# Kernel optimization log

Measured on AMD Instinct MI355X. Metric: run time of the kernel, lower is better.

The kernel has to match this reference:

```python
import jax, jax.numpy as jnp
import numpy as np

B, CIN, COUT, R = 8, 256, 256, 128  # H = W = R (required by the module's permute-then-conv structure)


def _init_linear(key, out_c, in_c):
    # mimic torch Conv2d(kernel=1) default init: uniform(-1/sqrt(fan_in), 1/sqrt(fan_in))
    k1, k2 = jax.random.split(key)
    bound = 1.0 / np.sqrt(in_c)
    W = jax.random.uniform(k1, (out_c, in_c), jnp.float32, -bound, bound)
    b = jax.random.uniform(k2, (out_c,), jnp.float32, -bound, bound)
    return W, b


def setup_inputs() -> dict:
    key = jax.random.key(0)
    keys = jax.random.split(key, 9)
    x = jax.random.normal(keys[0], (B, CIN, R, R), jnp.float32)
    Wr, br = _init_linear(keys[1], R, CIN)          # resize conv
    Wqw, bqw = _init_linear(keys[2], R, R)          # width-attn q (mixes over H axis, H==R)
    Wkw, bkw = _init_linear(keys[3], R, R)
    Wvw, bvw = _init_linear(keys[4], R, R)
    Wqh, bqh = _init_linear(keys[5], R, R)          # height-attn q (mixes over W axis, W==R)
    Wkh, bkh = _init_linear(keys[6], R, R)
    Wvh, bvh = _init_linear(keys[7], R, R)
    Wo, bo = _init_linear(keys[8], COUT, R)         # restore conv
    return dict(x=x, Wr=Wr, br=br, Wqw=Wqw, bqw=bqw, Wkw=Wkw, bkw=bkw, Wvw=Wvw, bvw=bvw,
                Wqh=Wqh, bqh=bqh, Wkh=Wkh, bkh=bkh, Wvh=Wvh, bvh=bvh, Wo=Wo, bo=bo)


def _csaa_forward(x, Wr, br, Wqw, bqw, Wkw, bkw, Wvw, bvw, Wqh, bqh, Wkh, bkh, Wvh, bvh, Wo, bo):
    # resize 1x1 conv: [B,CIN,H,W] -> [B,R,H,W]
    resized = jnp.einsum('oc,bchw->bohw', Wr, x) + br[None, :, None, None]

    # --- width-branch AxialAttention (height_dim=False) ---
    # permute(0,2,1,3): [B,R,H,W] -> [B,H,R,W]; 1x1 conv now mixes over the H axis (H==R)
    xp = jnp.transpose(resized, (0, 2, 1, 3))                      # [B,H,R,W]
    q = jnp.einsum('oh,bhrw->borw', Wqw, xp) + bqw[None, :, None, None]
    k = jnp.einsum('oh,bhrw->borw', Wkw, xp) + bkw[None, :, None, None]
    v = jnp.einsum('oh,bhrw->borw', Wvw, xp) + bvw[None, :, None, None]
    attn = jax.nn.softmax(jnp.einsum('borw,bouw->boru', q, k), axis=-1)  # [B,O,R,R]
    out = jnp.einsum('boru,bouw->borw', attn, v)                   # [B,O,R,W]
    w_attn = jnp.transpose(out, (0, 2, 1, 3))                      # [B,R,O,W] == [B,R,H,W]

    # --- height-branch AxialAttention (height_dim=True) ---
    # permute(0,3,1,2): [B,R,H,W] -> [B,W,R,H]; 1x1 conv mixes over the W axis (W==R)
    xp = jnp.transpose(w_attn, (0, 3, 1, 2))                       # [B,W,R,H]
    q = jnp.einsum('ow,bwrh->borh', Wqh, xp) + bqh[None, :, None, None]
    k = jnp.einsum('ow,bwrh->borh', Wkh, xp) + bkh[None, :, None, None]
    v = jnp.einsum('ow,bwrh->borh', Wvh, xp) + bvh[None, :, None, None]
    attn = jax.nn.softmax(jnp.einsum('borh,bouh->boru', q, k), axis=-1)  # [B,O,R,R]
    out = jnp.einsum('boru,bouh->borh', attn, v)                   # [B,O,R,H]
    h_attn = jnp.transpose(out, (0, 2, 3, 1))                      # [B,R,H,O] == [B,R,H,W]

    # restore 1x1 conv: [B,R,H,W] -> [B,COUT,H,W]
    return jnp.einsum('oc,bchw->bohw', Wo, h_attn) + bo[None, :, None, None]


def reference(x, Wr, br, Wqw, bqw, Wkw, bkw, Wvw, bvw, Wqh, bqh, Wkh, bkh, Wvh, bvh, Wo, bo):
    return _csaa_forward(x, Wr, br, Wqw, bqw, Wkw, bkw, Wvw, bvw,
                         Wqh, bqh, Wkh, bkh, Wvh, bvh, Wo, bo)
```

## Files before the change

kernel.cpp:

```cpp
#include <hip/hip_runtime.h>
#include <hip/hip_bf16.h>


typedef __attribute__((ext_vector_type(8))) short bf16x8;
typedef __attribute__((ext_vector_type(4))) float f32x4;

__device__ __forceinline__ short f2b(float f) {
    __hip_bfloat16 h = __float2bfloat16(f);
    short s; __builtin_memcpy(&s, &h, 2);
    return s;
}

__device__ __forceinline__ int swx(int row) { return (row ^ (row >> 3)) & 7; }
__device__ __forceinline__ int swzb(int row, int blk) {
    return (row << 7) + ((blk ^ swx(row)) << 3);
}

__device__ __forceinline__ void gload16(const void* g, void* l) {
    __builtin_amdgcn_global_load_lds(
        (const __attribute__((address_space(1))) void*)g,
        (__attribute__((address_space(3))) void*)l, 16, 0, 0);
}

__device__ __forceinline__ void mfma32x128(const short* __restrict__ SA,
                                           const short* __restrict__ SB,
                                           f32x4 (&acc)[2][8], int lane, int wr) {
    #pragma unroll
    for (int kk = 0; kk < 4; kk++) {
        const int kb = kk * 4 + (lane >> 4);
        bf16x8 a[2], b[8];
        #pragma unroll
        for (int mi = 0; mi < 2; mi++)
            a[mi] = *(const bf16x8*)&SA[swzb(wr + mi * 16 + (lane & 15), kb)];
        #pragma unroll
        for (int ni = 0; ni < 8; ni++)
            b[ni] = *(const bf16x8*)&SB[swzb(ni * 16 + (lane & 15), kb)];
        #pragma unroll
        for (int mi = 0; mi < 2; mi++)
            #pragma unroll
            for (int ni = 0; ni < 8; ni++)
                acc[mi][ni] = __builtin_amdgcn_mfma_f32_16x16x32_bf16(
                    a[mi], b[ni], acc[mi][ni], 0, 0, 0);
    }
}

__device__ __forceinline__ void mfma16x128(const short* __restrict__ SA,
                                           const short* __restrict__ SB,
                                           f32x4 (&acc)[8], int lane, int wr16) {
    #pragma unroll
    for (int kk = 0; kk < 4; kk++) {
        const int kb = kk * 4 + (lane >> 4);
        bf16x8 a = *(const bf16x8*)&SA[swzb(wr16 + (lane & 15), kb)];
        bf16x8 b[8];
        #pragma unroll
        for (int ni = 0; ni < 8; ni++)
            b[ni] = *(const bf16x8*)&SB[swzb(ni * 16 + (lane & 15), kb)];
        #pragma unroll
        for (int ni = 0; ni < 8; ni++)
            acc[ni] = __builtin_amdgcn_mfma_f32_16x16x32_bf16(
                a, b[ni], acc[ni], 0, 0, 0);
    }
}

__device__ __forceinline__ void stage_nf_bf16(const short* __restrict__ Bb,
                                              long long b_r, int k0,
                                              short* __restrict__ Bs, int t) {
    const int n8 = t & 15, kb = t >> 4;
    bf16x8 rk[8];
    #pragma unroll
    for (int i = 0; i < 8; i++)
        rk[i] = *(const bf16x8*)(Bb + (long long)(k0 + kb * 8 + i) * b_r + n8 * 8);
    #pragma unroll
    for (int j = 0; j < 8; j++) {
        bf16x8 col;
        #pragma unroll
        for (int i = 0; i < 8; i++) col[i] = rk[i][j];
        *(bf16x8*)&Bs[swzb(n8 * 8 + j, kb)] = col;
    }
}

__device__ __forceinline__ void stage_nf_f32(const float* __restrict__ Bb,
                                             long long b_r, int k0,
                                             short* __restrict__ Bs, int t) {
    const int n8 = t & 15, kb = t >> 4;
    bf16x8 rk[8];
    #pragma unroll
    for (int i = 0; i < 8; i++) {
        const float* s = Bb + (long long)(k0 + kb * 8 + i) * b_r + n8 * 8;
        float4 v0 = *(const float4*)s, v1 = *(const float4*)(s + 4);
        rk[i][0] = f2b(v0.x); rk[i][1] = f2b(v0.y);
        rk[i][2] = f2b(v0.z); rk[i][3] = f2b(v0.w);
        rk[i][4] = f2b(v1.x); rk[i][5] = f2b(v1.y);
        rk[i][6] = f2b(v1.z); rk[i][7] = f2b(v1.w);
    }
    #pragma unroll
    for (int j = 0; j < 8; j++) {
        bf16x8 col;
        #pragma unroll
        for (int i = 0; i < 8; i++) col[i] = rk[i][j];
        *(bf16x8*)&Bs[swzb(n8 * 8 + j, kb)] = col;
    }
}

__global__ __launch_bounds__(256)
void wprep(const float* __restrict__ Wr, const float* __restrict__ Wqw,
           const float* __restrict__ Wkw, const float* __restrict__ Wvw,
           const float* __restrict__ Wqh, const float* __restrict__ Wkh,
           const float* __restrict__ Wvh, const float* __restrict__ Wo,
           short* __restrict__ dst) {
    const int id = blockIdx.y;
    const float* W; int M, K, off;
    switch (id) {
        case 0: W = Wr;  M = 128; K = 256; off = 0;      break;
        case 1: W = Wqw; M = 128; K = 128; off = 32768;  break;
        case 2: W = Wkw; M = 128; K = 128; off = 49152;  break;
        case 3: W = Wvw; M = 128; K = 128; off = 65536;  break;
        case 4: W = Wqh; M = 128; K = 128; off = 81920;  break;
        case 5: W = Wkh; M = 128; K = 128; off = 98304;  break;
        case 6: W = Wvh; M = 128; K = 128; off = 114688; break;
        default: W = Wo; M = 256; K = 128; off = 131072; break;
    }
    int g = blockIdx.x * 256 + threadIdx.x;
    if (g >= (M * K) >> 3) return;
    int gpr = K >> 3;
    int row = g / gpr;
    int blk = g - row * gpr;
    int ks = blk >> 4, bi = blk & 15;
    int my = row >> 7, r = row & 127;
    int nks = K >> 7;
    const float* s = W + (long long)row * K + blk * 8;
    float4 v0 = *(const float4*)s, v1 = *(const float4*)(s + 4);
    bf16x8 ov;
    ov[0] = f2b(v0.x); ov[1] = f2b(v0.y); ov[2] = f2b(v0.z); ov[3] = f2b(v0.w);
    ov[4] = f2b(v1.x); ov[5] = f2b(v1.y); ov[6] = f2b(v1.z); ov[7] = f2b(v1.w);
    *(bf16x8*)(dst + off + (my * nks + ks) * 16384 + swzb(r, bi)) = ov;
}

__global__ __launch_bounds__(256)
void gemm_p1(const short* __restrict__ A0, const float* __restrict__ bias0,
             const float* __restrict__ Bsrc,
             long long b_z, long long b_x, long long b_r,
             short* __restrict__ C0,
             long long c_z, long long c_x, long long c_m) {
    __shared__ short As[16384];
    __shared__ short Bs[16384];
    const int t = threadIdx.x;
    const int lane = t & 63;
    const int wid = t >> 6;
    const int wr = wid * 32;
    const int bx = blockIdx.x, bz = blockIdx.z;

    f32x4 acc[2][8];
    #pragma unroll
    for (int mi = 0; mi < 2; mi++)
        #pragma unroll
        for (int ni = 0; ni < 8; ni++) acc[mi][ni] = (f32x4){0.f, 0.f, 0.f, 0.f};

    #pragma unroll
    for (int ks = 0; ks < 2; ks++) {
        if (ks) __syncthreads();
        stage_nf_f32(Bsrc + bz * b_z + bx * b_x, b_r, ks * 128, Bs, t);
        const short* Ai = A0 + ks * 16384;
        #pragma unroll
        for (int i = 0; i < 8; i++) {
            int q = wid * 8 + i;
            gload16(Ai + q * 512 + lane * 8, &As[q * 512]);
        }
        __syncthreads();
        mfma32x128(As, Bs, acc, lane, wr);
    }

    #pragma unroll
    for (int mi = 0; mi < 2; mi++)
        #pragma unroll
        for (int r = 0; r < 4; r++) {
            int row = wr + mi * 16 + (lane >> 4) * 4 + r;
            float bb = bias0[row];
            #pragma unroll
            for (int ni = 0; ni < 8; ni++) {
                int col = ni * 16 + (lane & 15);
                As[swzb(row, col >> 3) + (col & 7)] = f2b(acc[mi][ni][r] + bb);
            }
        }
    short* Cg = C0 + bz * c_z + bx * c_x;
    #pragma unroll
    for (int i = 0; i < 8; i++) {
        int idx = lane + i * 64;
        int row = wr + (idx >> 4), ch = idx & 15;
        *(bf16x8*)(Cg + (long long)row * c_m + ch * 8) =
            *(const bf16x8*)&As[swzb(row, ch)];
    }
}

template<int NW, int BMODE, bool F32OUT>
__global__ __launch_bounds__(256, 3)
void gemmw64(const short* __restrict__ A0, const short* __restrict__ A1,
             const short* __restrict__ A2,
             const float* __restrict__ bias0, const float* __restrict__ bias1,
             const float* __restrict__ bias2,
             const void* __restrict__ Bsrc, long long b_z, long long b_x,
             long long b_r,
             short* __restrict__ C0, short* __restrict__ C1,
             short* __restrict__ C2, float* __restrict__ Cf,
             long long c_z, long long c_x, long long c_m) {
    __shared__ short As[8192];
    __shared__ short Bs[16384];
    const int t = threadIdx.x;
    const int lane = t & 63;
    const int wid = t >> 6;
    const int wr16 = wid * 16;
    const int bx = blockIdx.x, my = blockIdx.y, bz = blockIdx.z;
    const int mbase = my * 64;

    if (BMODE == 0) {
        const short* Bb = (const short*)Bsrc + bz * b_z + bx * b_x;
        #pragma unroll
        for (int i = 0; i < 8; i++) {
            int q = wid * 8 + i;
            int row = q * 4 + (lane >> 4);
            gload16(Bb + (long long)row * b_r + (((lane & 15) ^ swx(row)) << 3),
                    &Bs[q * 512]);
        }
    } else {
        stage_nf_bf16((const short*)Bsrc + bz * b_z + bx * b_x, b_r, 0, Bs, t);
    }
    {
        const short* Ai = A0 + my * 8192;
        #pragma unroll
        for (int i = 0; i < 4; i++) {
            int q = wid * 4 + i;
            gload16(Ai + q * 512 + lane * 8, &As[q * 512]);
        }
    }
    __syncthreads();

    #pragma unroll
    for (int g = 0; g < NW; g++) {
        const float* bias = (g == 0) ? bias0 : (g == 1) ? bias1 : bias2;
        f32x4 acc[8];
        #pragma unroll
        for (int ni = 0; ni < 8; ni++) acc[ni] = (f32x4){0.f, 0.f, 0.f, 0.f};
        mfma16x128(As, Bs, acc, lane, wr16);

        if (F32OUT) {
            float* Cb = Cf + bz * c_z + bx * c_x;
            #pragma unroll
            for (int r = 0; r < 4; r++) {
                int row = mbase + wr16 + (lane >> 4) * 4 + r;
                float bb = bias[row];
                float* cp = Cb + (long long)row * c_m + (lane & 15);
                #pragma unroll
                for (int ni = 0; ni < 8; ni++)
                    cp[ni * 16] = acc[ni][r] + bb;
            }
        } else {
            #pragma unroll
            for (int r = 0; r < 4; r++) {
                int row = wr16 + (lane >> 4) * 4 + r;
                float bb = bias[mbase + row];
                #pragma unroll
                for (int ni = 0; ni < 8; ni++) {
                    int col = ni * 16 + (lane & 15);
                    As[swzb(row, col >> 3) + (col & 7)] = f2b(acc[ni][r] + bb);
                }
            }
            short* Cg = ((g == 0) ? C0 : (g == 1) ? C1 : C2)
                      + bz * c_z + bx * c_x;
            #pragma unroll
            for (int i = 0; i < 4; i++) {
                int idx = lane + i * 64;
                int row = wr16 + (idx >> 4), ch = idx & 15;
                *(bf16x8*)(Cg + (long long)(mbase + row) * c_m + ch * 8) =
                    *(const bf16x8*)&As[swzb(row, ch)];
            }
        }
        if (g + 1 < NW) {
            const short* Ai = ((g == 0) ? A1 : A2) + my * 8192;
            #pragma unroll
            for (int i = 0; i < 4; i++) {
                int q = wid * 4 + i;
                gload16(Ai + q * 512 + lane * 8, &As[q * 512]);
            }
            __syncthreads();
        }
    }
}

template<bool TEPI>
__global__ __launch_bounds__(256)
void attnk(const short* __restrict__ Q, const short* __restrict__ Kp,
           const short* __restrict__ V, short* __restrict__ O) {
    __shared__ short SA[16384];
    __shared__ short SB[16384];
    const int t = threadIdx.x;
    const int lane = t & 63;
    const int wid = t >> 6;
    const int wr = wid * 32;
    const long long poff = (long long)blockIdx.z * 2097152LL
                         + (long long)blockIdx.x * 16384LL;
    const short* Qb = Q + poff;
    const short* Kb = Kp + poff;
    const short* Vb = V + poff;
    short* Ob = O + (long long)blockIdx.z * 2097152LL + (long long)blockIdx.x * 128LL;

    #pragma unroll
    for (int i = 0; i < 8; i++) {
        int q = wid * 8 + i;
        int row = q * 4 + (lane >> 4);
        int sw = (((lane & 15) ^ swx(row)) << 3);
        gload16(Qb + row * 128 + sw, &SA[q * 512]);
        gload16(Kb + row * 128 + sw, &SB[q * 512]);
    }
    const int n8 = t & 15, kb = t >> 4;
    bf16x8 vk[8];
    #pragma unroll
    for (int i = 0; i < 8; i++)
        vk[i] = *(const bf16x8*)(Vb + (kb * 8 + i) * 128 + n8 * 8);
    __syncthreads();

    f32x4 acc[2][8];
    #pragma unroll
    for (int mi = 0; mi < 2; mi++)
        #pragma unroll
        for (int ni = 0; ni < 8; ni++) acc[mi][ni] = (f32x4){0.f, 0.f, 0.f, 0.f};
    mfma32x128(SA, SB, acc, lane, wr);

    float rs[2][4];
    #pragma unroll
    for (int mi = 0; mi < 2; mi++)
        #pragma unroll
        for (int r = 0; r < 4; r++) {
            float mx = acc[mi][0][r];
            #pragma unroll
            for (int ni = 1; ni < 8; ni++) mx = fmaxf(mx, acc[mi][ni][r]);
            #pragma unroll
            for (int d = 1; d < 16; d <<= 1) mx = fmaxf(mx, __shfl_xor(mx, d, 64));
            float s = 0.f;
            float p[8];
            #pragma unroll
            for (int ni = 0; ni < 8; ni++) {
                p[ni] = __expf(acc[mi][ni][r] - mx);
                s += p[ni];
            }
            #pragma unroll
            for (int d = 1; d < 16; d <<= 1) s += __shfl_xor(s, d, 64);
            rs[mi][r] = 1.f / s;
            int row = wr + mi * 16 + (lane >> 4) * 4 + r;
            #pragma unroll
            for (int ni = 0; ni < 8; ni++) {
                int col = ni * 16 + (lane & 15);
                SA[swzb(row, col >> 3) + (col & 7)] = f2b(p[ni]);
            }
        }
    __syncthreads();

    #pragma unroll
    for (int j = 0; j < 8; j++) {
        bf16x8 col;
        #pragma unroll
        for (int i = 0; i < 8; i++) col[i] = vk[i][j];
        *(bf16x8*)&SB[swzb(n8 * 8 + j, kb)] = col;
    }
    __syncthreads();

    f32x4 acc2[2][8];
    #pragma unroll
    for (int mi = 0; mi < 2; mi++)
        #pragma unroll
        for (int ni = 0; ni < 8; ni++) acc2[mi][ni] = (f32x4){0.f, 0.f, 0.f, 0.f};
    mfma32x128(SA, SB, acc2, lane, wr);

    if (!TEPI) {
        #pragma unroll
        for (int mi = 0; mi < 2; mi++)
            #pragma unroll
            for (int r = 0; r < 4; r++) {
                int row = wr + mi * 16 + (lane >> 4) * 4 + r;
                float rinv = rs[mi][r];
                #pragma unroll
                for (int ni = 0; ni < 8; ni++) {
                    int col = ni * 16 + (lane & 15);
                    SA[swzb(row, col >> 3) + (col & 7)] = f2b(acc2[mi][ni][r] * rinv);
                }
            }
        #pragma unroll
        for (int i = 0; i < 8; i++) {
            int idx = lane + i * 64;
            int row = wr + (idx >> 4), ch = idx & 15;
            *(bf16x8*)(Ob + (long long)row * 16384 + ch * 8) =
                *(const bf16x8*)&SA[swzb(row, ch)];
        }
    } else {
        __syncthreads();
        #pragma unroll
        for (int mi = 0; mi < 2; mi++)
            #pragma unroll
            for (int r = 0; r < 4; r++) {
                int row = wr + mi * 16 + (lane >> 4) * 4 + r;
                float rinv = rs[mi][r];
                #pragma unroll
                for (int ni = 0; ni < 8; ni++) {
                    int col = ni * 16 + (lane & 15);
                    SB[swzb(col, row >> 3) + (row & 7)] = f2b(acc2[mi][ni][r] * rinv);
                }
            }
        __syncthreads();
        #pragma unroll
        for (int i = 0; i < 8; i++) {
            int idx = t + i * 256;
            int row = idx >> 4, ch = idx & 15;
            *(bf16x8*)(Ob + (long long)row * 16384 + ch * 8) =
                *(const bf16x8*)&SB[swzb(row, ch)];
        }
    }
}

extern "C" void kernel_launch(void* const* d_in, const int* in_sizes, int n_in,
                              void* d_out, int out_size, void* d_ws, size_t ws_size,
                              hipStream_t stream) {
    const float* x   = (const float*)d_in[0];
    const float* Wr  = (const float*)d_in[1];
    const float* br  = (const float*)d_in[2];
    const float* Wqw = (const float*)d_in[3];
    const float* bqw = (const float*)d_in[4];
    const float* Wkw = (const float*)d_in[5];
    const float* bkw = (const float*)d_in[6];
    const float* Wvw = (const float*)d_in[7];
    const float* bvw = (const float*)d_in[8];
    const float* Wqh = (const float*)d_in[9];
    const float* bqh = (const float*)d_in[10];
    const float* Wkh = (const float*)d_in[11];
    const float* bkh = (const float*)d_in[12];
    const float* Wvh = (const float*)d_in[13];
    const float* bvh = (const float*)d_in[14];
    const float* Wo  = (const float*)d_in[15];
    const float* bo  = (const float*)d_in[16];
    float* out = (float*)d_out;
    (void)in_sizes; (void)n_in; (void)out_size; (void)ws_size;

    const long long U = 16777216LL;
    short* wsp = (short*)d_ws;
    short* s0 = wsp;
    short* s1 = wsp + U;
    short* s2 = wsp + 2 * U;
    short* s3 = wsp + 3 * U;
    short* wb = wsp + 4 * U;
    short* wWr  = wb;
    short* wWqw = wb + 32768;
    short* wWkw = wb + 49152;
    short* wWvw = wb + 65536;
    short* wWqh = wb + 81920;
    short* wWkh = wb + 98304;
    short* wWvh = wb + 114688;
    short* wWo  = wb + 131072;

    dim3 blk(256);

    wprep<<<dim3(16, 8), blk, 0, stream>>>(Wr, Wqw, Wkw, Wvw, Wqh, Wkh, Wvh, Wo, wb);

    gemm_p1<<<dim3(128, 1, 8), blk, 0, stream>>>(
        wWr, br, x, 4194304LL, 128LL, 16384LL,
        s0, 2097152LL, 128LL, 16384LL);

    gemmw64<3, 1, false><<<dim3(128, 2, 8), blk, 0, stream>>>(
        wWqw, wWkw, wWvw, bqw, bkw, bvw,
        s0, 2097152LL, 16384LL, 128LL,
        s1, s2, s3, nullptr, 2097152LL, 128LL, 16384LL);

    attnk<false><<<dim3(128, 1, 8), blk, 0, stream>>>(s1, s2, s3, s0);

    gemmw64<3, 0, false><<<dim3(128, 2, 8), blk, 0, stream>>>(
        wWqh, wWkh, wWvh, bqh, bkh, bvh,
        s0, 2097152LL, 16384LL, 128LL,
        s1, s2, s3, nullptr, 2097152LL, 128LL, 16384LL);

    attnk<true><<<dim3(128, 1, 8), blk, 0, stream>>>(s1, s2, s3, s0);

    gemmw64<1, 0, true><<<dim3(128, 4, 8), blk, 0, stream>>>(
        wWo, nullptr, nullptr, bo, nullptr, nullptr,
        s0, 2097152LL, 16384LL, 128LL,
        nullptr, nullptr, nullptr, out, 4194304LL, 128LL, 16384LL);
}
```

Before: 216.7 us.

## Read weights from global in MFMA fragment layout and split attention by query halves

Weights are pre-packed into an MFMA-fragment order so GEMM kernels load A operands directly from global/L2 into registers instead of staging them through LDS, halving LDS use and allowing higher occupancy (launch bounds 4). The QKV projection kernel now assigns one weight per grid-y block with a 128-row tile instead of looping over weights with 64-row tiles, and the output projection uses 128-row tiles. The first attention pass is replaced by a variant splitting queries into two 64-row halves for more blocks. Risks include uncoalesced global A loads and redundant K/V staging across query halves.

```diff
diff --git a/kernel.cpp b/kernel.cpp
--- a/kernel.cpp
+++ b/kernel.cpp
@@ -22,6 +22,54 @@
         (__attribute__((address_space(3))) void*)l, 16, 0, 0);
 }
 
+__device__ __forceinline__ void mfma_ag(const short* __restrict__ Ai,
+                                        const short* __restrict__ Bs,
+                                        f32x4 (&acc)[2][8], int lane, int wr) {
+    #pragma unroll
+    for (int kk = 0; kk < 4; kk++) {
+        const int kb = kk * 4 + (lane >> 4);
+        bf16x8 a[2];
+        #pragma unroll
+        for (int mi = 0; mi < 2; mi++)
+            a[mi] = *(const bf16x8*)(Ai + kb * 1024
+                                        + (wr + mi * 16 + (lane & 15)) * 8);
+        #pragma unroll
+        for (int nh = 0; nh < 2; nh++) {
+            bf16x8 b[4];
+            #pragma unroll
+            for (int nj = 0; nj < 4; nj++)
+                b[nj] = *(const bf16x8*)&Bs[swzb((nh * 4 + nj) * 16 + (lane & 15), kb)];
+            #pragma unroll
+            for (int mi = 0; mi < 2; mi++)
+                #pragma unroll
+                for (int nj = 0; nj < 4; nj++)
+                    acc[mi][nh * 4 + nj] = __builtin_amdgcn_mfma_f32_16x16x32_bf16(
+                        a[mi], b[nj], acc[mi][nh * 4 + nj], 0, 0, 0);
+        }
+    }
+}
+
+__device__ __forceinline__ void mfma16x128(const short* __restrict__ SA,
+                                           const short* __restrict__ SB,
+                                           f32x4 (&acc)[8], int lane, int wr16) {
+    #pragma unroll
+    for (int kk = 0; kk < 4; kk++) {
+        const int kb = kk * 4 + (lane >> 4);
+        bf16x8 a = *(const bf16x8*)&SA[swzb(wr16 + (lane & 15), kb)];
+        #pragma unroll
+        for (int nh = 0; nh < 2; nh++) {
+            bf16x8 b[4];
+            #pragma unroll
+            for (int nj = 0; nj < 4; nj++)
+                b[nj] = *(const bf16x8*)&SB[swzb((nh * 4 + nj) * 16 + (lane & 15), kb)];
+            #pragma unroll
+            for (int nj = 0; nj < 4; nj++)
+                acc[nh * 4 + nj] = __builtin_amdgcn_mfma_f32_16x16x32_bf16(
+                    a, b[nj], acc[nh * 4 + nj], 0, 0, 0);
+        }
+    }
+}
+
 __device__ __forceinline__ void mfma32x128(const short* __restrict__ SA,
                                            const short* __restrict__ SB,
                                            f32x4 (&acc)[2][8], int lane, int wr) {
@@ -41,24 +89,6 @@
             for (int ni = 0; ni < 8; ni++)
                 acc[mi][ni] = __builtin_amdgcn_mfma_f32_16x16x32_bf16(
                     a[mi], b[ni], acc[mi][ni], 0, 0, 0);
-    }
-}
-
-__device__ __forceinline__ void mfma16x128(const short* __restrict__ SA,
-                                           const short* __restrict__ SB,
-                                           f32x4 (&acc)[8], int lane, int wr16) {
-    #pragma unroll
-    for (int kk = 0; kk < 4; kk++) {
-        const int kb = kk * 4 + (lane >> 4);
-        bf16x8 a = *(const bf16x8*)&SA[swzb(wr16 + (lane & 15), kb)];
-        bf16x8 b[8];
-        #pragma unroll
-        for (int ni = 0; ni < 8; ni++)
-            b[ni] = *(const bf16x8*)&SB[swzb(ni * 16 + (lane & 15), kb)];
-        #pragma unroll
-        for (int ni = 0; ni < 8; ni++)
-            acc[ni] = __builtin_amdgcn_mfma_f32_16x16x32_bf16(
-                a, b[ni], acc[ni], 0, 0, 0);
     }
 }
 
@@ -125,7 +155,7 @@
     int gpr = K >> 3;
     int row = g / gpr;
     int blk = g - row * gpr;
-    int ks = blk >> 4, bi = blk & 15;
+    int ks = blk >> 4, kb = blk & 15;
     int my = row >> 7, r = row & 127;
     int nks = K >> 7;
     const float* s = W + (long long)row * K + blk * 8;
@@ -133,16 +163,15 @@
     bf16x8 ov;
     ov[0] = f2b(v0.x); ov[1] = f2b(v0.y); ov[2] = f2b(v0.z); ov[3] = f2b(v0.w);
     ov[4] = f2b(v1.x); ov[5] = f2b(v1.y); ov[6] = f2b(v1.z); ov[7] = f2b(v1.w);
-    *(bf16x8*)(dst + off + (my * nks + ks) * 16384 + swzb(r, bi)) = ov;
-}
-
-__global__ __launch_bounds__(256)
+    *(bf16x8*)(dst + off + ((my * nks + ks) * 16 + kb) * 1024 + r * 8) = ov;
+}
+
+__global__ __launch_bounds__(256, 4)
 void gemm_p1(const short* __restrict__ A0, const float* __restrict__ bias0,
              const float* __restrict__ Bsrc,
              long long b_z, long long b_x, long long b_r,
              short* __restrict__ C0,
              long long c_z, long long c_x, long long c_m) {
-    __shared__ short As[16384];
     __shared__ short Bs[16384];
     const int t = threadIdx.x;
     const int lane = t & 63;
@@ -160,15 +189,10 @@
     for (int ks = 0; ks < 2; ks++) {
         if (ks) __syncthreads();
         stage_nf_f32(Bsrc + bz * b_z + bx * b_x, b_r, ks * 128, Bs, t);
-        const short* Ai = A0 + ks * 16384;
-        #pragma unroll
-        for (int i = 0; i < 8; i++) {
-            int q = wid * 8 + i;
-            gload16(Ai + q * 512 + lane * 8, &As[q * 512]);
-        }
         __syncthreads();
-        mfma32x128(As, Bs, acc, lane, wr);
-    }
+        mfma_ag(A0 + ks * 16384, Bs, acc, lane, wr);
+    }
+    __syncthreads();
 
     #pragma unroll
     for (int mi = 0; mi < 2; mi++)
@@ -179,7 +203,7 @@
             #pragma unroll
             for (int ni = 0; ni < 8; ni++) {
                 int col = ni * 16 + (lane & 15);
-                As[swzb(row, col >> 3) + (col & 7)] = f2b(acc[mi][ni][r] + bb);
+                Bs[swzb(row, col >> 3) + (col & 7)] = f2b(acc[mi][ni][r] + bb);
             }
         }
     short* Cg = C0 + bz * c_z + bx * c_x;
@@ -188,29 +212,40 @@
         int idx = lane + i * 64;
         int row = wr + (idx >> 4), ch = idx & 15;
         *(bf16x8*)(Cg + (long long)row * c_m + ch * 8) =
-            *(const bf16x8*)&As[swzb(row, ch)];
+            *(const bf16x8*)&Bs[swzb(row, ch)];
     }
 }
 
 template<int NW, int BMODE, bool F32OUT>
-__global__ __launch_bounds__(256, 3)
-void gemmw64(const short* __restrict__ A0, const short* __restrict__ A1,
-             const short* __restrict__ A2,
-             const float* __restrict__ bias0, const float* __restrict__ bias1,
-             const float* __restrict__ bias2,
-             const void* __restrict__ Bsrc, long long b_z, long long b_x,
-             long long b_r,
-             short* __restrict__ C0, short* __restrict__ C1,
-             short* __restrict__ C2, float* __restrict__ Cf,
-             long long c_z, long long c_x, long long c_m) {
-    __shared__ short As[8192];
+__global__ __launch_bounds__(256, 4)
+void gemmu(const short* __restrict__ A0, const short* __restrict__ A1,
+           const short* __restrict__ A2,
+           const float* __restrict__ bias0, const float* __restrict__ bias1,
+           const float* __restrict__ bias2,
+           const void* __restrict__ Bsrc, long long b_z, long long b_x,
+           long long b_r,
+           short* __restrict__ C0, short* __restrict__ C1,
+           short* __restrict__ C2, float* __restrict__ Cf,
+           long long c_z, long long c_x, long long c_m) {
     __shared__ short Bs[16384];
     const int t = threadIdx.x;
     const int lane = t & 63;
     const int wid = t >> 6;
-    const int wr16 = wid * 16;
-    const int bx = blockIdx.x, my = blockIdx.y, bz = blockIdx.z;
-    const int mbase = my * 64;
+    const int wr = wid * 32;
+    const int bx = blockIdx.x, gy = blockIdx.y, bz = blockIdx.z;
+
+    const short* Ai;
+    const float* bias;
+    int myoff;
+    if (NW > 1) {
+        Ai = (gy == 0) ? A0 : (gy == 1) ? A1 : A2;
+        bias = (gy == 0) ? bias0 : (gy == 1) ? bias1 : bias2;
+        myoff = 0;
+    } else {
+        Ai = A0 + gy * 16384;
+        bias = bias0;
+        myoff = gy * 128;
+    }
 
     if (BMODE == 0) {
         const short* Bb = (const short*)Bsrc + bz * b_z + bx * b_x;
@@ -224,65 +259,151 @@
     } else {
         stage_nf_bf16((const short*)Bsrc + bz * b_z + bx * b_x, b_r, 0, Bs, t);
     }
-    {
-        const short* Ai = A0 + my * 8192;
-        #pragma unroll
-        for (int i = 0; i < 4; i++) {
-            int q = wid * 4 + i;
-            gload16(Ai + q * 512 + lane * 8, &As[q * 512]);
-        }
-    }
-    __syncthreads();
-
-    #pragma unroll
-    for (int g = 0; g < NW; g++) {
-        const float* bias = (g == 0) ? bias0 : (g == 1) ? bias1 : bias2;
-        f32x4 acc[8];
-        #pragma unroll
-        for (int ni = 0; ni < 8; ni++) acc[ni] = (f32x4){0.f, 0.f, 0.f, 0.f};
-        mfma16x128(As, Bs, acc, lane, wr16);
-
-        if (F32OUT) {
-            float* Cb = Cf + bz * c_z + bx * c_x;
+    __syncthreads();
+
+    f32x4 acc[2][8];
+    #pragma unroll
+    for (int mi = 0; mi < 2; mi++)
+        #pragma unroll
+        for (int ni = 0; ni < 8; ni++) acc[mi][ni] = (f32x4){0.f, 0.f, 0.f, 0.f};
+    mfma_ag(Ai, Bs, acc, lane, wr);
+
+    if (F32OUT) {
+        float* Cb = Cf + bz * c_z + bx * c_x;
+        #pragma unroll
+        for (int mi = 0; mi < 2; mi++)
             #pragma unroll
             for (int r = 0; r < 4; r++) {
-                int row = mbase + wr16 + (lane >> 4) * 4 + r;
+                int row = myoff + wr + mi * 16 + (lane >> 4) * 4 + r;
                 float bb = bias[row];
                 float* cp = Cb + (long long)row * c_m + (lane & 15);
                 #pragma unroll
                 for (int ni = 0; ni < 8; ni++)
-                    cp[ni * 16] = acc[ni][r] + bb;
+                    cp[ni * 16] = acc[mi][ni][r] + bb;
             }
-        } else {
+    } else {
+        __syncthreads();
+        #pragma unroll
+        for (int mi = 0; mi < 2; mi++)
             #pragma unroll
             for (int r = 0; r < 4; r++) {
-                int row = wr16 + (lane >> 4) * 4 + r;
-                float bb = bias[mbase + row];
+                int row = wr + mi * 16 + (lane >> 4) * 4 + r;
+                float bb = bias[row];
                 #pragma unroll
                 for (int ni = 0; ni < 8; ni++) {
                     int col = ni * 16 + (lane & 15);
-                    As[swzb(row, col >> 3) + (col & 7)] = f2b(acc[ni][r] + bb);
+                    Bs[swzb(row, col >> 3) + (col & 7)] = f2b(acc[mi][ni][r] + bb);
                 }
             }
-            short* Cg = ((g == 0) ? C0 : (g == 1) ? C1 : C2)
-                      + bz * c_z + bx * c_x;
-            #pragma unroll
-            for (int i = 0; i < 4; i++) {
-                int idx = lane + i * 64;
-                int row = wr16 + (idx >> 4), ch = idx & 15;
-                *(bf16x8*)(Cg + (long long)(mbase + row) * c_m + ch * 8) =
-                    *(const bf16x8*)&As[swzb(row, ch)];
-            }
-        }
-        if (g + 1 < NW) {
-            const short* Ai = ((g == 0) ? A1 : A2) + my * 8192;
-            #pragma unroll
-            for (int i = 0; i < 4; i++) {
-                int q = wid * 4 + i;
-                gload16(Ai + q * 512 + lane * 8, &As[q * 512]);
-            }
-            __syncthreads();
-        }
+        short* Cg = ((NW > 1) ? ((gy == 0) ? C0 : (gy == 1) ? C1 : C2) : C0)
+                  + bz * c_z + bx * c_x;
+        #pragma unroll
+        for (int i = 0; i < 8; i++) {
+            int idx = lane + i * 64;
+            int row = wr + (idx >> 4), ch = idx & 15;
+            *(bf16x8*)(Cg + (long long)row * c_m + ch * 8) =
+                *(const bf16x8*)&Bs[swzb(row, ch)];
+        }
+    }
+}
+
+__global__ __launch_bounds__(256, 3)
+void attnq(const short* __restrict__ Q, const short* __restrict__ Kp,
+           const short* __restrict__ V, short* __restrict__ O) {
+    __shared__ short SA[8192];
+    __shared__ short SB[16384];
+    const int t = threadIdx.x;
+    const int lane = t & 63;
+    const int wid = t >> 6;
+    const int wr16 = wid * 16;
+    const int o = blockIdx.x, qh = blockIdx.y, b = blockIdx.z;
+    const long long poff = (long long)b * 2097152LL + (long long)o * 16384LL;
+    const short* Qb = Q + poff + qh * 64 * 128;
+    const short* Kb = Kp + poff;
+    const short* Vb = V + poff;
+    short* Ob = O + (long long)b * 2097152LL + (long long)o * 128LL
+              + (long long)qh * 64 * 16384LL;
+
+    #pragma unroll
+    for (int i = 0; i < 4; i++) {
+        int q = wid * 4 + i;
+        int row = q * 4 + (lane >> 4);
+        gload16(Qb + row * 128 + (((lane & 15) ^ swx(row)) << 3), &SA[q * 512]);
+    }
+    #pragma unroll
+    for (int i = 0; i < 8; i++) {
+        int q = wid * 8 + i;
+        int row = q * 4 + (lane >> 4);
+        gload16(Kb + row * 128 + (((lane & 15) ^ swx(row)) << 3), &SB[q * 512]);
+    }
+    const int n8 = t & 15, kb8 = t >> 4;
+    bf16x8 vk[8];
+    #pragma unroll
+    for (int i = 0; i < 8; i++)
+        vk[i] = *(const bf16x8*)(Vb + (kb8 * 8 + i) * 128 + n8 * 8);
+    __syncthreads();
+
+    f32x4 acc[8];
+    #pragma unroll
+    for (int ni = 0; ni < 8; ni++) acc[ni] = (f32x4){0.f, 0.f, 0.f, 0.f};
+    mfma16x128(SA, SB, acc, lane, wr16);
+
+    float rs[4];
+    #pragma unroll
+    for (int r = 0; r < 4; r++) {
+        float mx = acc[0][r];
+        #pragma unroll
+        for (int ni = 1; ni < 8; ni++) mx = fmaxf(mx, acc[ni][r]);
+        #pragma unroll
+        for (int d = 1; d < 16; d <<= 1) mx = fmaxf(mx, __shfl_xor(mx, d, 64));
+        float s = 0.f, p[8];
+        #pragma unroll
+        for (int ni = 0; ni < 8; ni++) {
+            p[ni] = __expf(acc[ni][r] - mx);
+            s += p[ni];
+        }
+        #pragma unroll
+        for (int d = 1; d < 16; d <<= 1) s += __shfl_xor(s, d, 64);
+        rs[r] = 1.f / s;
+        int row = wr16 + (lane >> 4) * 4 + r;
+        #pragma unroll
+        for (int ni = 0; ni < 8; ni++) {
+            int col = ni * 16 + (lane & 15);
+            SA[swzb(row, col >> 3) + (col & 7)] = f2b(p[ni]);
+        }
+    }
+    __syncthreads();
+
+    #pragma unroll
+    for (int j = 0; j < 8; j++) {
+        bf16x8 col;
+        #pragma unroll
+        for (int i = 0; i < 8; i++) col[i] = vk[i][j];
+        *(bf16x8*)&SB[swzb(n8 * 8 + j, kb8)] = col;
+    }
+    __syncthreads();
+
+    f32x4 acc2[8];
+    #pragma unroll
+    for (int ni = 0; ni < 8; ni++) acc2[ni] = (f32x4){0.f, 0.f, 0.f, 0.f};
+    mfma16x128(SA, SB, acc2, lane, wr16);
+
+    #pragma unroll
+    for (int r = 0; r < 4; r++) {
+        int row = wr16 + (lane >> 4) * 4 + r;
+        float rinv = rs[r];
+        #pragma unroll
+        for (int ni = 0; ni < 8; ni++) {
+            int col = ni * 16 + (lane & 15);
+            SA[swzb(row, col >> 3) + (col & 7)] = f2b(acc2[ni][r] * rinv);
+        }
+    }
+    #pragma unroll
+    for (int i = 0; i < 4; i++) {
+        int idx = lane + i * 64;
+        int row = wr16 + (idx >> 4), ch = idx & 15;
+        *(bf16x8*)(Ob + (long long)row * 16384 + ch * 8) =
+            *(const bf16x8*)&SA[swzb(row, ch)];
     }
 }
 
@@ -335,8 +456,7 @@
             for (int ni = 1; ni < 8; ni++) mx = fmaxf(mx, acc[mi][ni][r]);
             #pragma unroll
             for (int d = 1; d < 16; d <<= 1) mx = fmaxf(mx, __shfl_xor(mx, d, 64));
-            float s = 0.f;
-            float p[8];
+            float s = 0.f, p[8];
             #pragma unroll
             for (int ni = 0; ni < 8; ni++) {
                 p[ni] = __expf(acc[mi][ni][r] - mx);
@@ -462,21 +582,21 @@
         wWr, br, x, 4194304LL, 128LL, 16384LL,
         s0, 2097152LL, 128LL, 16384LL);
 
-    gemmw64<3, 1, false><<<dim3(128, 2, 8), blk, 0, stream>>>(
+    gemmu<3, 1, false><<<dim3(128, 3, 8), blk, 0, stream>>>(
         wWqw, wWkw, wWvw, bqw, bkw, bvw,
         s0, 2097152LL, 16384LL, 128LL,
         s1, s2, s3, nullptr, 2097152LL, 128LL, 16384LL);
 
-    attnk<false><<<dim3(128, 1, 8), blk, 0, stream>>>(s1, s2, s3, s0);
-
-    gemmw64<3, 0, false><<<dim3(128, 2, 8), blk, 0, stream>>>(
+    attnq<<<dim3(128, 2, 8), blk, 0, stream>>>(s1, s2, s3, s0);
+
+    gemmu<3, 0, false><<<dim3(128, 3, 8), blk, 0, stream>>>(
         wWqh, wWkh, wWvh, bqh, bkh, bvh,
         s0, 2097152LL, 16384LL, 128LL,
         s1, s2, s3, nullptr, 2097152LL, 128LL, 16384LL);
 
     attnk<true><<<dim3(128, 1, 8), blk, 0, stream>>>(s1, s2, s3, s0);
 
-    gemmw64<1, 0, true><<<dim3(128, 4, 8), blk, 0, stream>>>(
+    gemmu<1, 0, true><<<dim3(128, 2, 8), blk, 0, stream>>>(
         wWo, nullptr, nullptr, bo, nullptr, nullptr,
         s0, 2097152LL, 16384LL, 128LL,
         nullptr, nullptr, nullptr, out, 4194304LL, 128LL, 16384LL);
```

Result: slower. 224.0 us (+3.4%).
